# Kernel optimization log

Hardware: AMD Instinct MI355X
Metric: run time of the kernel (lower is better)

The kernel has to match this reference:

```python
import jax, jax.numpy as jnp
import numpy as np

B, D, H, K, V, M = 64, 4096, 32, 128, 128, 4096


def setup_inputs() -> dict:
    key = jax.random.key(0)
    ks = jax.random.split(key, 7)
    return {
        "x": jax.random.normal(ks[0], (B, D), dtype=jnp.float32),
        "prev_K": jax.random.normal(ks[1], (B, M, K), dtype=jnp.float32),
        "prev_V": jax.random.normal(ks[2], (B, M, V), dtype=jnp.float32),
        "P_q": jax.random.normal(ks[3], (H, D, K), dtype=jnp.float32),
        "P_k": jax.random.normal(ks[4], (D, K), dtype=jnp.float32),
        "P_v": jax.random.normal(ks[5], (D, V), dtype=jnp.float32),
        "P_o": jax.random.normal(ks[6], (H, D, V), dtype=jnp.float32),
    }


def reference(x, prev_K, prev_V, P_q, P_k, P_v, P_o):
    # Per-head query projection: [b,d] x [h,d,k] -> [b,h,k]
    q = jnp.einsum('bd,hdk->bhk', x, P_q)
    # Single shared K/V head (multi-query): append new token to cache along m
    new_k = jnp.einsum('bd,dk->bk', x, P_k)  # [b,k]
    new_v = jnp.einsum('bd,dv->bv', x, P_v)  # [b,v]
    Kc = jnp.concatenate([prev_K, new_k[:, None, :]], axis=1)  # [b,m+1,k]
    Vc = jnp.concatenate([prev_V, new_v[:, None, :]], axis=1)  # [b,m+1,v]
    # Attention over cache
    logits = jnp.einsum('bhk,bmk->bhm', q, Kc)
    weights = jax.nn.softmax(logits, axis=-1)
    O = jnp.einsum('bhm,bmv->bhv', weights, Vc)
    # Output projection: [b,h,v] x [h,d,v] -> [b,d]
    y = jnp.einsum('bhv,hdv->bd', O, P_o)
    return (y, Kc, Vc)
```

## Files before the change

### kernel.cpp

```cpp
#include <hip/hip_runtime.h>
#include <math.h>

#define Bb 64
#define Dd 4096
#define Hh 32
#define Kk 128
#define Vv 128
#define Mm 4096
#define MC 4097
#define NCH 16
#define NSLOT 17

#define WS_K1P  0
#define WS_Q    4456448
#define WS_NEWK (WS_Q + Bb*Hh*Kk)
#define WS_NEWV (WS_NEWK + Bb*Kk)
#define WS_PM   (WS_NEWV + Bb*Vv)
#define WS_PL   (WS_PM + Bb*NSLOT*Hh)
#define WS_PO   (WS_PL + Bb*NSLOT*Hh)
#define WS_O    (WS_PO + Bb*NSLOT*Hh*Vv)
#define WS_YP   (WS_O + Bb*Hh*Vv)

#define YSLOT (Bb*Dd)

#define OUT_Y  0
#define OUT_KC (Bb*Dd)
#define OUT_VC (OUT_KC + Bb*MC*Kk)

__global__ __launch_bounds__(256) void k1A_proj(const float* __restrict__ x,
        const float* __restrict__ Pq, const float* __restrict__ Pk,
        const float* __restrict__ Pv, float* __restrict__ part) {
    const int hidx = blockIdx.x;
    const int d0c  = blockIdx.y * 256;
    const int t = threadIdx.x;
    const int kg = t & 15, bg = t >> 4;
    const int kd = kg * 4, b0 = bg * 4;

    const float* P;
    if (hidx < Hh)       P = Pq + (size_t)hidx * Dd * Kk;
    else if (hidx == Hh) P = Pk;
    else                 P = Pv;

    __shared__ float xs[32 * 65];
    __shared__ float ps[32 * 128];

    float acc[4][8];
    #pragma unroll
    for (int a = 0; a < 4; a++)
        #pragma unroll
        for (int c = 0; c < 8; c++) acc[a][c] = 0.f;

    for (int tt = 0; tt < 8; tt++) {
        const int d0 = d0c + tt * 32;
        #pragma unroll
        for (int ii = 0; ii < 8; ii++) {
            int f = ii * 256 + t;
            int i = f & 31, bb = f >> 5;
            xs[i * 65 + bb] = x[(size_t)bb * Dd + d0 + i];
        }
        #pragma unroll
        for (int ii = 0; ii < 4; ii++) {
            int f = ii * 256 + t;
            int i = f >> 5, k4 = (f & 31) * 4;
            *(float4*)&ps[i * 128 + k4] = *(const float4*)&P[(size_t)(d0 + i) * Kk + k4];
        }
        __syncthreads();
        #pragma unroll
        for (int i = 0; i < 32; i++) {
            float xb[4];
            #pragma unroll
            for (int a = 0; a < 4; a++) xb[a] = xs[i * 65 + b0 + a];
            float4 p0 = *(float4*)&ps[i * 128 + kd];
            float4 p1 = *(float4*)&ps[i * 128 + 64 + kd];
            float pp[8] = {p0.x, p0.y, p0.z, p0.w, p1.x, p1.y, p1.z, p1.w};
            #pragma unroll
            for (int a = 0; a < 4; a++)
                #pragma unroll
                for (int c = 0; c < 8; c++)
                    acc[a][c] = fmaf(xb[a], pp[c], acc[a][c]);
        }
        __syncthreads();
    }
    float* dst = part + ((size_t)hidx * 16 + blockIdx.y) * 8192;
    #pragma unroll
    for (int a = 0; a < 4; a++) {
        int b = b0 + a;
        *(float4*)&dst[b * 128 + kd]      = make_float4(acc[a][0], acc[a][1], acc[a][2], acc[a][3]);
        *(float4*)&dst[b * 128 + 64 + kd] = make_float4(acc[a][4], acc[a][5], acc[a][6], acc[a][7]);
    }
}

__global__ __launch_bounds__(256) void k1B_reduce(const float* __restrict__ part,
        float* __restrict__ ws) {
    const int o = blockIdx.x * 256 + threadIdx.x;
    const int hidx = o >> 13;
    const int rest = o & 8191;
    float s = 0.f;
    #pragma unroll
    for (int c = 0; c < 16; c++) s += part[((size_t)hidx * 16 + c) * 8192 + rest];
    if (hidx < Hh) {
        int b = rest >> 7, k = rest & 127;
        ws[WS_Q + ((size_t)b * Hh + hidx) * Kk + k] = s;
    } else if (hidx == Hh) {
        ws[WS_NEWK + rest] = s;
    } else {
        ws[WS_NEWV + rest] = s;
    }
}

__global__ __launch_bounds__(256) void kflash(const float* __restrict__ prevK,
        const float* __restrict__ prevV, const float* __restrict__ wq,
        float* __restrict__ outKc, float* __restrict__ outVc,
        float* __restrict__ PM, float* __restrict__ PL, float* __restrict__ PO) {
    const int c = blockIdx.x;
    const int b = blockIdx.y;
    const int t = threadIdx.x;
    const int hg = t >> 4, lg = t & 15;
    const int h2 = hg * 2;

    __shared__ float ks_t[64 * 64];
    __shared__ float vs[64 * 132];
    __shared__ float qs[128 * 34];
    __shared__ float wl_t[64 * 36];

    {
        const int h = t >> 3, kc = t & 7;
        const float* qr = wq + ((size_t)b * Hh + h) * Kk + kc * 16;
        float4 a0 = *(const float4*)&qr[0];
        float4 a1 = *(const float4*)&qr[4];
        float4 a2 = *(const float4*)&qr[8];
        float4 a3 = *(const float4*)&qr[12];
        const int k0 = kc * 16;
        qs[(k0+ 0)*34 + h] = a0.x; qs[(k0+ 1)*34 + h] = a0.y;
        qs[(k0+ 2)*34 + h] = a0.z; qs[(k0+ 3)*34 + h] = a0.w;
        qs[(k0+ 4)*34 + h] = a1.x; qs[(k0+ 5)*34 + h] = a1.y;
        qs[(k0+ 6)*34 + h] = a1.z; qs[(k0+ 7)*34 + h] = a1.w;
        qs[(k0+ 8)*34 + h] = a2.x; qs[(k0+ 9)*34 + h] = a2.y;
        qs[(k0+10)*34 + h] = a2.z; qs[(k0+11)*34 + h] = a2.w;
        qs[(k0+12)*34 + h] = a3.x; qs[(k0+13)*34 + h] = a3.y;
        qs[(k0+14)*34 + h] = a3.z; qs[(k0+15)*34 + h] = a3.w;
    }

    float rm[2] = {-3.0e38f, -3.0e38f};
    float rl[2] = {0.f, 0.f};
    float accO[2][8] = {};
    const int kq = t & 15;
    const int vq = t & 31;

    for (int st = 0; st < 4; st++) {
        const int m0 = c * 256 + st * 64;
        __syncthreads();
        float4 kreg[8], vreg[8];
        #pragma unroll
        for (int ii = 0; ii < 4; ii++) {
            int mm = (t >> 4) + ii * 16;
            const float* src = prevK + ((size_t)b * Mm + m0 + mm) * Kk + kq * 4;
            kreg[ii]     = *(const float4*)src;
            kreg[ii + 4] = *(const float4*)(src + 64);
        }
        #pragma unroll
        for (int ii = 0; ii < 8; ii++) {
            int mm = (t >> 5) + ii * 8;
            vreg[ii] = *(const float4*)(prevV + ((size_t)b * Mm + m0 + mm) * Vv + vq * 4);
        }
        #pragma unroll
        for (int ii = 0; ii < 4; ii++) {
            int mm = (t >> 4) + ii * 16;
            int cs = (mm + 4 * kq) & 63;
            ks_t[(kq*4+0)*64 + cs] = kreg[ii].x;
            ks_t[(kq*4+1)*64 + cs] = kreg[ii].y;
            ks_t[(kq*4+2)*64 + cs] = kreg[ii].z;
            ks_t[(kq*4+3)*64 + cs] = kreg[ii].w;
        }
        #pragma unroll
        for (int ii = 0; ii < 8; ii++) {
            int mm = (t >> 5) + ii * 8;
            *(float4*)&vs[mm * 132 + vq * 4] = vreg[ii];
        }
        __syncthreads();
        #pragma unroll
        for (int ii = 0; ii < 4; ii++) {
            int mm = (t >> 4) + ii * 16;
            float* dstK = outKc + ((size_t)b * MC + m0 + mm) * Kk + kq * 4;
            *(float4*)dstK        = kreg[ii];
            *(float4*)(dstK + 64) = kreg[ii + 4];
        }
        #pragma unroll
        for (int ii = 0; ii < 8; ii++) {
            int mm = (t >> 5) + ii * 8;
            *(float4*)(outVc + ((size_t)b * MC + m0 + mm) * Vv + vq * 4) = vreg[ii];
        }
        float s[2][4] = {};
        #pragma unroll 4
        for (int k = 0; k < 64; k++) {
            float2 q2 = *(float2*)&qs[k * 34 + h2];
            float4 k4 = *(float4*)&ks_t[k * 64 + ((4*lg + 4*(k>>2)) & 63)];
            s[0][0] = fmaf(q2.x, k4.x, s[0][0]); s[0][1] = fmaf(q2.x, k4.y, s[0][1]);
            s[0][2] = fmaf(q2.x, k4.z, s[0][2]); s[0][3] = fmaf(q2.x, k4.w, s[0][3]);
            s[1][0] = fmaf(q2.y, k4.x, s[1][0]); s[1][1] = fmaf(q2.y, k4.y, s[1][1]);
            s[1][2] = fmaf(q2.y, k4.z, s[1][2]); s[1][3] = fmaf(q2.y, k4.w, s[1][3]);
        }
        __syncthreads();
        #pragma unroll
        for (int ii = 0; ii < 4; ii++) {
            int mm = (t >> 4) + ii * 16;
            int cs = (mm + 4 * kq) & 63;
            ks_t[(kq*4+0)*64 + cs] = kreg[ii+4].x;
            ks_t[(kq*4+1)*64 + cs] = kreg[ii+4].y;
            ks_t[(kq*4+2)*64 + cs] = kreg[ii+4].z;
            ks_t[(kq*4+3)*64 + cs] = kreg[ii+4].w;
        }
        __syncthreads();
        #pragma unroll 4
        for (int k = 0; k < 64; k++) {
            float2 q2 = *(float2*)&qs[(64 + k) * 34 + h2];
            float4 k4 = *(float4*)&ks_t[k * 64 + ((4*lg + 4*(k>>2)) & 63)];
            s[0][0] = fmaf(q2.x, k4.x, s[0][0]); s[0][1] = fmaf(q2.x, k4.y, s[0][1]);
            s[0][2] = fmaf(q2.x, k4.z, s[0][2]); s[0][3] = fmaf(q2.x, k4.w, s[0][3]);
            s[1][0] = fmaf(q2.y, k4.x, s[1][0]); s[1][1] = fmaf(q2.y, k4.y, s[1][1]);
            s[1][2] = fmaf(q2.y, k4.z, s[1][2]); s[1][3] = fmaf(q2.y, k4.w, s[1][3]);
        }
        float al[2];
        #pragma unroll
        for (int a = 0; a < 2; a++) {
            float mloc = fmaxf(fmaxf(s[a][0], s[a][1]), fmaxf(s[a][2], s[a][3]));
            mloc = fmaxf(mloc, __shfl_xor(mloc, 1, 64));
            mloc = fmaxf(mloc, __shfl_xor(mloc, 2, 64));
            mloc = fmaxf(mloc, __shfl_xor(mloc, 4, 64));
            mloc = fmaxf(mloc, __shfl_xor(mloc, 8, 64));
            float nm = fmaxf(rm[a], mloc);
            al[a] = __expf(rm[a] - nm);
            float psum = 0.f;
            #pragma unroll
            for (int cc = 0; cc < 4; cc++) {
                float p = __expf(s[a][cc] - nm);
                wl_t[(4*lg + cc) * 36 + h2 + a] = p;
                psum += p;
            }
            psum += __shfl_xor(psum, 1, 64);
            psum += __shfl_xor(psum, 2, 64);
            psum += __shfl_xor(psum, 4, 64);
            psum += __shfl_xor(psum, 8, 64);
            rl[a] = rl[a] * al[a] + psum;
            rm[a] = nm;
        }
        #pragma unroll
        for (int a = 0; a < 2; a++)
            #pragma unroll
            for (int j = 0; j < 8; j++) accO[a][j] *= al[a];
        for (int mm = 0; mm < 64; mm++) {
            float2 w2 = *(float2*)&wl_t[mm * 36 + h2];
            float4 v0 = *(float4*)&vs[mm * 132 + 4 * lg];
            float4 v1 = *(float4*)&vs[mm * 132 + 64 + 4 * lg];
            accO[0][0] = fmaf(w2.x, v0.x, accO[0][0]);
            accO[0][1] = fmaf(w2.x, v0.y, accO[0][1]);
            accO[0][2] = fmaf(w2.x, v0.z, accO[0][2]);
            accO[0][3] = fmaf(w2.x, v0.w, accO[0][3]);
            accO[0][4] = fmaf(w2.x, v1.x, accO[0][4]);
            accO[0][5] = fmaf(w2.x, v1.y, accO[0][5]);
            accO[0][6] = fmaf(w2.x, v1.z, accO[0][6]);
            accO[0][7] = fmaf(w2.x, v1.w, accO[0][7]);
            accO[1][0] = fmaf(w2.y, v0.x, accO[1][0]);
            accO[1][1] = fmaf(w2.y, v0.y, accO[1][1]);
            accO[1][2] = fmaf(w2.y, v0.z, accO[1][2]);
            accO[1][3] = fmaf(w2.y, v0.w, accO[1][3]);
            accO[1][4] = fmaf(w2.y, v1.x, accO[1][4]);
            accO[1][5] = fmaf(w2.y, v1.y, accO[1][5]);
            accO[1][6] = fmaf(w2.y, v1.z, accO[1][6]);
            accO[1][7] = fmaf(w2.y, v1.w, accO[1][7]);
        }
    }
    const size_t base = ((size_t)b * NSLOT + c) * Hh;
    if (lg == 0) {
        PM[base + h2]     = rm[0];
        PM[base + h2 + 1] = rm[1];
        PL[base + h2]     = rl[0];
        PL[base + h2 + 1] = rl[1];
    }
    #pragma unroll
    for (int a = 0; a < 2; a++) {
        float* po = PO + (base + h2 + a) * Vv;
        *(float4*)&po[4*lg]      = make_float4(accO[a][0], accO[a][1], accO[a][2], accO[a][3]);
        *(float4*)&po[64 + 4*lg] = make_float4(accO[a][4], accO[a][5], accO[a][6], accO[a][7]);
    }
}

__global__ __launch_bounds__(128) void knew(const float* __restrict__ ws,
        float* __restrict__ outKc, float* __restrict__ outVc,
        float* __restrict__ PM, float* __restrict__ PL, float* __restrict__ PO) {
    const int b = blockIdx.x, t = threadIdx.x;
    const float* q    = ws + WS_Q;
    const float* newk = ws + WS_NEWK;
    const float* newv = ws + WS_NEWV;
    const int h = t >> 2, j = t & 3;
    const float* qr = q + ((size_t)b * Hh + h) * Kk + j * 32;
    const float* nk = newk + (size_t)b * Kk + j * 32;
    float s0 = 0.f, s1 = 0.f, s2 = 0.f, s3 = 0.f;
    #pragma unroll
    for (int i = 0; i < 8; i++) {
        float4 a  = *(const float4*)&qr[i * 4];
        float4 c4 = *(const float4*)&nk[i * 4];
        s0 = fmaf(a.x, c4.x, s0); s1 = fmaf(a.y, c4.y, s1);
        s2 = fmaf(a.z, c4.z, s2); s3 = fmaf(a.w, c4.w, s3);
    }
    float s = (s0 + s1) + (s2 + s3);
    s += __shfl_xor(s, 1, 64);
    s += __shfl_xor(s, 2, 64);
    const size_t base = ((size_t)b * NSLOT + 16) * Hh;
    if (j == 0) { PM[base + h] = s; PL[base + h] = 1.f; }
    float nv = newv[(size_t)b * Vv + t];
    outKc[((size_t)b * MC + Mm) * Kk + t] = newk[(size_t)b * Kk + t];
    outVc[((size_t)b * MC + Mm) * Vv + t] = nv;
    #pragma unroll 4
    for (int hh = 0; hh < Hh; hh++)
        PO[(base + hh) * Vv + t] = nv;
}

__global__ __launch_bounds__(128) void kcomb(const float* __restrict__ PM,
        const float* __restrict__ PL, const float* __restrict__ PO,
        float* __restrict__ O) {
    const int h = blockIdx.x, b = blockIdx.y, t = threadIdx.x;
    __shared__ float ml[NSLOT], ll[NSLOT];
    if (t < NSLOT) {
        ml[t] = PM[((size_t)b * NSLOT + t) * Hh + h];
        ll[t] = PL[((size_t)b * NSLOT + t) * Hh + h];
    }
    __syncthreads();
    float M = -3.0e38f;
    #pragma unroll
    for (int c = 0; c < NSLOT; c++) M = fmaxf(M, ml[c]);
    float L = 0.f, o = 0.f;
    #pragma unroll
    for (int c = 0; c < NSLOT; c++) {
        float e = __expf(ml[c] - M);
        L += ll[c] * e;
        o = fmaf(e, PO[(((size_t)b * NSLOT + c) * Hh + h) * Vv + t], o);
    }
    O[((size_t)b * Hh + h) * Vv + t] = o / L;
}

__global__ __launch_bounds__(256) void k5_outproj(const float* __restrict__ O,
        const float* __restrict__ Po, float* __restrict__ ypart) {
    const int dbase = blockIdx.x * 64;
    const int hq = blockIdx.y;
    const int t = threadIdx.x;
    __shared__ float os[64 * 64];
    __shared__ float ps2[64 * 64];
    const int dg = t & 15, bg = t >> 4;
    const int d0 = dg * 4, b0 = bg * 4;
    float acc[4][4] = {};
    for (int hi = 0; hi < 4; hi++) {
        const int h = hq * 4 + hi;
        for (int vh = 0; vh < 2; vh++) {
            __syncthreads();
            #pragma unroll
            for (int ii = 0; ii < 4; ii++) {
                int f = ii * 256 + t;
                int vq2 = f & 15, r = f >> 4;
                int colp = (4 * vq2 + 4 * (r >> 2)) & 63;
                *(float4*)&os[r * 64 + colp] =
                    *(const float4*)&O[((size_t)(r * Hh + h)) * Vv + vh * 64 + 4 * vq2];
// ... 67 lines not shown
```

Baseline: 252.9 us.

## Double-buffer K/V register prefetch in flash kernel and halve chunk count

Each flash block now processes 512 cache rows in eight stages instead of 256 rows in four. The stage loop is fully unrolled through macros with two register buffers, so the next stage's K/V global loads are issued while the current stage computes. Launch bounds request two blocks per SM, and the partial-slot count drops from 17 to 9, which shrinks the combine work. The costs are higher register pressure, possible spills from holding two float4[8] buffers per thread, and half as many blocks (64x8), which lowers parallelism across the GPU.

```diff
diff --git a/kernel.cpp b/kernel.cpp
--- a/kernel.cpp
+++ b/kernel.cpp
@@ -8,8 +8,8 @@
 #define Vv 128
 #define Mm 4096
 #define MC 4097
-#define NCH 16
-#define NSLOT 17
+#define NCH 8
+#define NSLOT 9
 
 #define WS_K1P  0
 #define WS_Q    4456448
@@ -108,7 +108,133 @@
     }
 }
 
-__global__ __launch_bounds__(256) void kflash(const float* __restrict__ prevK,
+#define LOADKV(ST, KR, VR) { \
+    const int m0_ = c * 512 + (ST) * 64; \
+    _Pragma("unroll") \
+    for (int ii = 0; ii < 4; ii++) { \
+        int mm = mK + ii * 16; \
+        const float* src = prevK + ((size_t)b * Mm + m0_ + mm) * Kk + kq * 4; \
+        KR[ii]     = *(const float4*)src; \
+        KR[ii + 4] = *(const float4*)(src + 64); \
+    } \
+    _Pragma("unroll") \
+    for (int ii = 0; ii < 8; ii++) { \
+        int mm = mV + ii * 8; \
+        VR[ii] = *(const float4*)(prevV + ((size_t)b * Mm + m0_ + mm) * Vv + vq * 4); \
+    } }
+
+#define FLASH_BODY(KC, VC, KN, VN, ST, PRE) { \
+    const int m0_ = c * 512 + (ST) * 64; \
+    __syncthreads();                          \
+    _Pragma("unroll") \
+    for (int ii = 0; ii < 4; ii++) {          \
+        int mm = mK + ii * 16; \
+        int cs = (mm + 4 * kq) & 63; \
+        ks_t[(kq*4+0)*64 + cs] = KC[ii].x; \
+        ks_t[(kq*4+1)*64 + cs] = KC[ii].y; \
+        ks_t[(kq*4+2)*64 + cs] = KC[ii].z; \
+        ks_t[(kq*4+3)*64 + cs] = KC[ii].w; \
+    } \
+    _Pragma("unroll") \
+    for (int ii = 0; ii < 8; ii++) {          \
+        int mm = mV + ii * 8; \
+        *(float4*)&vs[mm * 132 + vq * 4] = VC[ii]; \
+    } \
+    __syncthreads();                          \
+    if (PRE) LOADKV((ST) + 1, KN, VN);        \
+    _Pragma("unroll") \
+    for (int ii = 0; ii < 4; ii++) {          \
+        int mm = mK + ii * 16; \
+        float* dK = outKc + ((size_t)b * MC + m0_ + mm) * Kk + kq * 4; \
+        *(float4*)dK        = KC[ii]; \
+        *(float4*)(dK + 64) = KC[ii + 4]; \
+    } \
+    _Pragma("unroll") \
+    for (int ii = 0; ii < 8; ii++) {          \
+        int mm = mV + ii * 8; \
+        *(float4*)(outVc + ((size_t)b * MC + m0_ + mm) * Vv + vq * 4) = VC[ii]; \
+    } \
+    float s[2][4] = {{0.f,0.f,0.f,0.f},{0.f,0.f,0.f,0.f}}; \
+    _Pragma("unroll 4") \
+    for (int k = 0; k < 64; k++) {            \
+        float2 q2 = *(float2*)&qs[k * 34 + h2]; \
+        float4 k4 = *(float4*)&ks_t[k * 64 + ((4*lg + 4*(k>>2)) & 63)]; \
+        s[0][0] = fmaf(q2.x, k4.x, s[0][0]); s[0][1] = fmaf(q2.x, k4.y, s[0][1]); \
+        s[0][2] = fmaf(q2.x, k4.z, s[0][2]); s[0][3] = fmaf(q2.x, k4.w, s[0][3]); \
+        s[1][0] = fmaf(q2.y, k4.x, s[1][0]); s[1][1] = fmaf(q2.y, k4.y, s[1][1]); \
+        s[1][2] = fmaf(q2.y, k4.z, s[1][2]); s[1][3] = fmaf(q2.y, k4.w, s[1][3]); \
+    } \
+    __syncthreads();                          \
+    _Pragma("unroll") \
+    for (int ii = 0; ii < 4; ii++) {          \
+        int mm = mK + ii * 16; \
+        int cs = (mm + 4 * kq) & 63; \
+        ks_t[(kq*4+0)*64 + cs] = KC[ii+4].x; \
+        ks_t[(kq*4+1)*64 + cs] = KC[ii+4].y; \
+        ks_t[(kq*4+2)*64 + cs] = KC[ii+4].z; \
+        ks_t[(kq*4+3)*64 + cs] = KC[ii+4].w; \
+    } \
+    __syncthreads();                          \
+    _Pragma("unroll 4") \
+    for (int k = 0; k < 64; k++) {            \
+        float2 q2 = *(float2*)&qs[(64 + k) * 34 + h2]; \
+        float4 k4 = *(float4*)&ks_t[k * 64 + ((4*lg + 4*(k>>2)) & 63)]; \
+        s[0][0] = fmaf(q2.x, k4.x, s[0][0]); s[0][1] = fmaf(q2.x, k4.y, s[0][1]); \
+        s[0][2] = fmaf(q2.x, k4.z, s[0][2]); s[0][3] = fmaf(q2.x, k4.w, s[0][3]); \
+        s[1][0] = fmaf(q2.y, k4.x, s[1][0]); s[1][1] = fmaf(q2.y, k4.y, s[1][1]); \
+        s[1][2] = fmaf(q2.y, k4.z, s[1][2]); s[1][3] = fmaf(q2.y, k4.w, s[1][3]); \
+    } \
+    float al[2]; \
+    _Pragma("unroll") \
+    for (int a = 0; a < 2; a++) {             \
+        float mloc = fmaxf(fmaxf(s[a][0], s[a][1]), fmaxf(s[a][2], s[a][3])); \
+        mloc = fmaxf(mloc, __shfl_xor(mloc, 1, 64)); \
+        mloc = fmaxf(mloc, __shfl_xor(mloc, 2, 64)); \
+        mloc = fmaxf(mloc, __shfl_xor(mloc, 4, 64)); \
+        mloc = fmaxf(mloc, __shfl_xor(mloc, 8, 64)); \
+        float nm = fmaxf(rm[a], mloc); \
+        al[a] = __expf(rm[a] - nm); \
+        float psum = 0.f; \
+        _Pragma("unroll") \
+        for (int cc = 0; cc < 4; cc++) { \
+            float p = __expf(s[a][cc] - nm); \
+            wl_t[(4*lg + cc) * 36 + h2 + a] = p; \
+            psum += p; \
+        } \
+        psum += __shfl_xor(psum, 1, 64); \
+        psum += __shfl_xor(psum, 2, 64); \
+        psum += __shfl_xor(psum, 4, 64); \
+        psum += __shfl_xor(psum, 8, 64); \
+        rl[a] = rl[a] * al[a] + psum; \
+        rm[a] = nm; \
+    } \
+    _Pragma("unroll") \
+    for (int a = 0; a < 2; a++) \
+        _Pragma("unroll") \
+        for (int j = 0; j < 8; j++) accO[a][j] *= al[a]; \
+    for (int mm = 0; mm < 64; mm++) {         \
+        float2 w2 = *(float2*)&wl_t[mm * 36 + h2]; \
+        float4 v0 = *(float4*)&vs[mm * 132 + 4 * lg]; \
+        float4 v1 = *(float4*)&vs[mm * 132 + 64 + 4 * lg]; \
+        accO[0][0] = fmaf(w2.x, v0.x, accO[0][0]); \
+        accO[0][1] = fmaf(w2.x, v0.y, accO[0][1]); \
+        accO[0][2] = fmaf(w2.x, v0.z, accO[0][2]); \
+        accO[0][3] = fmaf(w2.x, v0.w, accO[0][3]); \
+        accO[0][4] = fmaf(w2.x, v1.x, accO[0][4]); \
+        accO[0][5] = fmaf(w2.x, v1.y, accO[0][5]); \
+        accO[0][6] = fmaf(w2.x, v1.z, accO[0][6]); \
+        accO[0][7] = fmaf(w2.x, v1.w, accO[0][7]); \
+        accO[1][0] = fmaf(w2.y, v0.x, accO[1][0]); \
+        accO[1][1] = fmaf(w2.y, v0.y, accO[1][1]); \
+        accO[1][2] = fmaf(w2.y, v0.z, accO[1][2]); \
+        accO[1][3] = fmaf(w2.y, v0.w, accO[1][3]); \
+        accO[1][4] = fmaf(w2.y, v1.x, accO[1][4]); \
+        accO[1][5] = fmaf(w2.y, v1.y, accO[1][5]); \
+        accO[1][6] = fmaf(w2.y, v1.z, accO[1][6]); \
+        accO[1][7] = fmaf(w2.y, v1.w, accO[1][7]); \
+    } }
+
+__global__ __launch_bounds__(256, 2) void kflash(const float* __restrict__ prevK,
         const float* __restrict__ prevV, const float* __restrict__ wq,
         float* __restrict__ outKc, float* __restrict__ outVc,
         float* __restrict__ PM, float* __restrict__ PL, float* __restrict__ PO) {
@@ -117,11 +243,18 @@
     const int t = threadIdx.x;
     const int hg = t >> 4, lg = t & 15;
     const int h2 = hg * 2;
+    const int kq = t & 15;
+    const int mK = t >> 4;
+    const int vq = t & 31;
+    const int mV = t >> 5;
 
     __shared__ float ks_t[64 * 64];
     __shared__ float vs[64 * 132];
     __shared__ float qs[128 * 34];
     __shared__ float wl_t[64 * 36];
+
+    float4 ka[8], va[8], kb[8], vb[8];
+    LOADKV(0, ka, va);
 
     {
         const int h = t >> 3, kc = t & 7;
@@ -144,132 +277,16 @@
     float rm[2] = {-3.0e38f, -3.0e38f};
     float rl[2] = {0.f, 0.f};
     float accO[2][8] = {};
-    const int kq = t & 15;
-    const int vq = t & 31;
-
-    for (int st = 0; st < 4; st++) {
-        const int m0 = c * 256 + st * 64;
-        __syncthreads();
-        float4 kreg[8], vreg[8];
-        #pragma unroll
-        for (int ii = 0; ii < 4; ii++) {
-            int mm = (t >> 4) + ii * 16;
-            const float* src = prevK + ((size_t)b * Mm + m0 + mm) * Kk + kq * 4;
-            kreg[ii]     = *(const float4*)src;
-            kreg[ii + 4] = *(const float4*)(src + 64);
-        }
-        #pragma unroll
-        for (int ii = 0; ii < 8; ii++) {
-            int mm = (t >> 5) + ii * 8;
-            vreg[ii] = *(const float4*)(prevV + ((size_t)b * Mm + m0 + mm) * Vv + vq * 4);
-        }
-        #pragma unroll
-        for (int ii = 0; ii < 4; ii++) {
-            int mm = (t >> 4) + ii * 16;
-            int cs = (mm + 4 * kq) & 63;
-            ks_t[(kq*4+0)*64 + cs] = kreg[ii].x;
-            ks_t[(kq*4+1)*64 + cs] = kreg[ii].y;
-            ks_t[(kq*4+2)*64 + cs] = kreg[ii].z;
-            ks_t[(kq*4+3)*64 + cs] = kreg[ii].w;
-        }
-        #pragma unroll
-        for (int ii = 0; ii < 8; ii++) {
-            int mm = (t >> 5) + ii * 8;
-            *(float4*)&vs[mm * 132 + vq * 4] = vreg[ii];
-        }
-        __syncthreads();
-        #pragma unroll
-        for (int ii = 0; ii < 4; ii++) {
-            int mm = (t >> 4) + ii * 16;
-            float* dstK = outKc + ((size_t)b * MC + m0 + mm) * Kk + kq * 4;
-            *(float4*)dstK        = kreg[ii];
-            *(float4*)(dstK + 64) = kreg[ii + 4];
-        }
-        #pragma unroll
-        for (int ii = 0; ii < 8; ii++) {
-            int mm = (t >> 5) + ii * 8;
-            *(float4*)(outVc + ((size_t)b * MC + m0 + mm) * Vv + vq * 4) = vreg[ii];
-        }
-        float s[2][4] = {};
-        #pragma unroll 4
-        for (int k = 0; k < 64; k++) {
-            float2 q2 = *(float2*)&qs[k * 34 + h2];
-            float4 k4 = *(float4*)&ks_t[k * 64 + ((4*lg + 4*(k>>2)) & 63)];
-            s[0][0] = fmaf(q2.x, k4.x, s[0][0]); s[0][1] = fmaf(q2.x, k4.y, s[0][1]);
-            s[0][2] = fmaf(q2.x, k4.z, s[0][2]); s[0][3] = fmaf(q2.x, k4.w, s[0][3]);
-            s[1][0] = fmaf(q2.y, k4.x, s[1][0]); s[1][1] = fmaf(q2.y, k4.y, s[1][1]);
-            s[1][2] = fmaf(q2.y, k4.z, s[1][2]); s[1][3] = fmaf(q2.y, k4.w, s[1][3]);
-        }
-        __syncthreads();
-        #pragma unroll
-        for (int ii = 0; ii < 4; ii++) {
-            int mm = (t >> 4) + ii * 16;
-            int cs = (mm + 4 * kq) & 63;
-            ks_t[(kq*4+0)*64 + cs] = kreg[ii+4].x;
-            ks_t[(kq*4+1)*64 + cs] = kreg[ii+4].y;
-            ks_t[(kq*4+2)*64 + cs] = kreg[ii+4].z;
-            ks_t[(kq*4+3)*64 + cs] = kreg[ii+4].w;
-        }
-        __syncthreads();
-        #pragma unroll 4
-        for (int k = 0; k < 64; k++) {
-            float2 q2 = *(float2*)&qs[(64 + k) * 34 + h2];
-            float4 k4 = *(float4*)&ks_t[k * 64 + ((4*lg + 4*(k>>2)) & 63)];
-            s[0][0] = fmaf(q2.x, k4.x, s[0][0]); s[0][1] = fmaf(q2.x, k4.y, s[0][1]);
-            s[0][2] = fmaf(q2.x, k4.z, s[0][2]); s[0][3] = fmaf(q2.x, k4.w, s[0][3]);
-            s[1][0] = fmaf(q2.y, k4.x, s[1][0]); s[1][1] = fmaf(q2.y, k4.y, s[1][1]);
-            s[1][2] = fmaf(q2.y, k4.z, s[1][2]); s[1][3] = fmaf(q2.y, k4.w, s[1][3]);
-        }
-        float al[2];
-        #pragma unroll
-        for (int a = 0; a < 2; a++) {
-            float mloc = fmaxf(fmaxf(s[a][0], s[a][1]), fmaxf(s[a][2], s[a][3]));
-            mloc = fmaxf(mloc, __shfl_xor(mloc, 1, 64));
-            mloc = fmaxf(mloc, __shfl_xor(mloc, 2, 64));
-            mloc = fmaxf(mloc, __shfl_xor(mloc, 4, 64));
-            mloc = fmaxf(mloc, __shfl_xor(mloc, 8, 64));
-            float nm = fmaxf(rm[a], mloc);
-            al[a] = __expf(rm[a] - nm);
-            float psum = 0.f;
-            #pragma unroll
-            for (int cc = 0; cc < 4; cc++) {
-                float p = __expf(s[a][cc] - nm);
-                wl_t[(4*lg + cc) * 36 + h2 + a] = p;
-                psum += p;
-            }
-            psum += __shfl_xor(psum, 1, 64);
-            psum += __shfl_xor(psum, 2, 64);
-            psum += __shfl_xor(psum, 4, 64);
-            psum += __shfl_xor(psum, 8, 64);
-            rl[a] = rl[a] * al[a] + psum;
-            rm[a] = nm;
-        }
-        #pragma unroll
-        for (int a = 0; a < 2; a++)
-            #pragma unroll
-            for (int j = 0; j < 8; j++) accO[a][j] *= al[a];
-        for (int mm = 0; mm < 64; mm++) {
-            float2 w2 = *(float2*)&wl_t[mm * 36 + h2];
-            float4 v0 = *(float4*)&vs[mm * 132 + 4 * lg];
-            float4 v1 = *(float4*)&vs[mm * 132 + 64 + 4 * lg];
-            accO[0][0] = fmaf(w2.x, v0.x, accO[0][0]);
-            accO[0][1] = fmaf(w2.x, v0.y, accO[0][1]);
-            accO[0][2] = fmaf(w2.x, v0.z, accO[0][2]);
-            accO[0][3] = fmaf(w2.x, v0.w, accO[0][3]);
-            accO[0][4] = fmaf(w2.x, v1.x, accO[0][4]);
-            accO[0][5] = fmaf(w2.x, v1.y, accO[0][5]);
-            accO[0][6] = fmaf(w2.x, v1.z, accO[0][6]);
-            accO[0][7] = fmaf(w2.x, v1.w, accO[0][7]);
-            accO[1][0] = fmaf(w2.y, v0.x, accO[1][0]);
-            accO[1][1] = fmaf(w2.y, v0.y, accO[1][1]);
-            accO[1][2] = fmaf(w2.y, v0.z, accO[1][2]);
-            accO[1][3] = fmaf(w2.y, v0.w, accO[1][3]);
-            accO[1][4] = fmaf(w2.y, v1.x, accO[1][4]);
-            accO[1][5] = fmaf(w2.y, v1.y, accO[1][5]);
-            accO[1][6] = fmaf(w2.y, v1.z, accO[1][6]);
-            accO[1][7] = fmaf(w2.y, v1.w, accO[1][7]);
-        }
-    }
+
+    FLASH_BODY(ka, va, kb, vb, 0, true)
+    FLASH_BODY(kb, vb, ka, va, 1, true)
+    FLASH_BODY(ka, va, kb, vb, 2, true)
+    FLASH_BODY(kb, vb, ka, va, 3, true)
+    FLASH_BODY(ka, va, kb, vb, 4, true)
+    FLASH_BODY(kb, vb, ka, va, 5, true)
+    FLASH_BODY(ka, va, kb, vb, 6, true)
+    FLASH_BODY(kb, vb, ka, va, 7, false)
+
     const size_t base = ((size_t)b * NSLOT + c) * Hh;
     if (lg == 0) {
         PM[base + h2]     = rm[0];
@@ -306,7 +323,7 @@
     float s = (s0 + s1) + (s2 + s3);
     s += __shfl_xor(s, 1, 64);
     s += __shfl_xor(s, 2, 64);
-    const size_t base = ((size_t)b * NSLOT + 16) * Hh;
+    const size_t base = ((size_t)b * NSLOT + NCH) * Hh;
     if (j == 0) { PM[base + h] = s; PL[base + h] = 1.f; }
     float nv = newv[(size_t)b * Vv + t];
     outKc[((size_t)b * MC + Mm) * Kk + t] = newk[(size_t)b * Kk + t];
```

Result: slower. 287.5 us (+13.7%).

## Halve kflash LDS tiles and stage K/V in 32-row chunks for occupancy

Applied to the files above, without the earlier changes.

The K and V shared-memory staging buffers in kflash shrink to half size. K is now staged as four 32-wide k slices, each followed by its partial QK dot product, and V as two 32-row halves, each followed by its partial PV accumulation. Launch bounds now request 3 blocks per SM. The aim is to cut LDS use per block so more blocks stay resident and hide global memory latency. In exchange, each 64-row step gets several extra __syncthreads barriers, and register pressure under the stricter launch bound may cause spills.

```diff
diff --git a/kernel.cpp b/kernel.cpp
--- a/kernel.cpp
+++ b/kernel.cpp
@@ -108,7 +108,57 @@
     }
 }
 
-__global__ __launch_bounds__(256) void kflash(const float* __restrict__ prevK,
+
+#define WRITEK(SEL, OFF) { \
+    if ((kq >> 3) == (SEL)) { \
+        const int kq7 = kq & 7; \
+        _Pragma("unroll") \
+        for (int ii = 0; ii < 4; ii++) { \
+            int mm = mK + ii * 16; \
+            int cs = (mm + 4 * kq7) & 63; \
+            ks_t[(4*kq7+0)*64 + cs] = ka[ii+(OFF)].x; \
+            ks_t[(4*kq7+1)*64 + cs] = ka[ii+(OFF)].y; \
+            ks_t[(4*kq7+2)*64 + cs] = ka[ii+(OFF)].z; \
+            ks_t[(4*kq7+3)*64 + cs] = ka[ii+(OFF)].w; \
+        } \
+    } }
+
+#define QKQ(KB) { \
+    _Pragma("unroll 8") \
+    for (int r = 0; r < 32; r++) { \
+        float2 q2 = *(float2*)&qs[((KB) + r) * 34 + h2]; \
+        float4 k4 = *(float4*)&ks_t[r * 64 + ((4*lg + 4*(r>>2)) & 63)]; \
+        s[0][0] = fmaf(q2.x, k4.x, s[0][0]); s[0][1] = fmaf(q2.x, k4.y, s[0][1]); \
+        s[0][2] = fmaf(q2.x, k4.z, s[0][2]); s[0][3] = fmaf(q2.x, k4.w, s[0][3]); \
+        s[1][0] = fmaf(q2.y, k4.x, s[1][0]); s[1][1] = fmaf(q2.y, k4.y, s[1][1]); \
+        s[1][2] = fmaf(q2.y, k4.z, s[1][2]); s[1][3] = fmaf(q2.y, k4.w, s[1][3]); \
+    } }
+
+#define PVH(MB) { \
+    _Pragma("unroll 4") \
+    for (int mm = 0; mm < 32; mm++) { \
+        float2 w2 = *(float2*)&wl_t[((MB) + mm) * 36 + h2]; \
+        float4 v0 = *(float4*)&vs[mm * 132 + 4 * lg]; \
+        float4 v1 = *(float4*)&vs[mm * 132 + 64 + 4 * lg]; \
+        accO[0][0] = fmaf(w2.x, v0.x, accO[0][0]); \
+        accO[0][1] = fmaf(w2.x, v0.y, accO[0][1]); \
+        accO[0][2] = fmaf(w2.x, v0.z, accO[0][2]); \
+        accO[0][3] = fmaf(w2.x, v0.w, accO[0][3]); \
+        accO[0][4] = fmaf(w2.x, v1.x, accO[0][4]); \
+        accO[0][5] = fmaf(w2.x, v1.y, accO[0][5]); \
+        accO[0][6] = fmaf(w2.x, v1.z, accO[0][6]); \
+        accO[0][7] = fmaf(w2.x, v1.w, accO[0][7]); \
+        accO[1][0] = fmaf(w2.y, v0.x, accO[1][0]); \
+        accO[1][1] = fmaf(w2.y, v0.y, accO[1][1]); \
+        accO[1][2] = fmaf(w2.y, v0.z, accO[1][2]); \
+        accO[1][3] = fmaf(w2.y, v0.w, accO[1][3]); \
+        accO[1][4] = fmaf(w2.y, v1.x, accO[1][4]); \
+        accO[1][5] = fmaf(w2.y, v1.y, accO[1][5]); \
+        accO[1][6] = fmaf(w2.y, v1.z, accO[1][6]); \
+        accO[1][7] = fmaf(w2.y, v1.w, accO[1][7]); \
+    } }
+
+__global__ __launch_bounds__(256, 3) void kflash(const float* __restrict__ prevK,
         const float* __restrict__ prevV, const float* __restrict__ wq,
         float* __restrict__ outKc, float* __restrict__ outVc,
         float* __restrict__ PM, float* __restrict__ PL, float* __restrict__ PO) {
@@ -117,9 +167,13 @@
     const int t = threadIdx.x;
     const int hg = t >> 4, lg = t & 15;
     const int h2 = hg * 2;
-
-    __shared__ float ks_t[64 * 64];
-    __shared__ float vs[64 * 132];
+    const int kq = t & 15;
+    const int mK = t >> 4;
+    const int vq = t & 31;
+    const int mV = t >> 5;
+
+    __shared__ float ks_t[32 * 64];
+    __shared__ float vs[32 * 132];
     __shared__ float qs[128 * 34];
     __shared__ float wl_t[64 * 36];
 
@@ -144,82 +198,54 @@
     float rm[2] = {-3.0e38f, -3.0e38f};
     float rl[2] = {0.f, 0.f};
     float accO[2][8] = {};
-    const int kq = t & 15;
-    const int vq = t & 31;
 
     for (int st = 0; st < 4; st++) {
         const int m0 = c * 256 + st * 64;
         __syncthreads();
-        float4 kreg[8], vreg[8];
+        float4 ka[8], va[8];
         #pragma unroll
         for (int ii = 0; ii < 4; ii++) {
-            int mm = (t >> 4) + ii * 16;
+            int mm = mK + ii * 16;
             const float* src = prevK + ((size_t)b * Mm + m0 + mm) * Kk + kq * 4;
-            kreg[ii]     = *(const float4*)src;
-            kreg[ii + 4] = *(const float4*)(src + 64);
+            ka[ii]     = *(const float4*)src;
+            ka[ii + 4] = *(const float4*)(src + 64);
         }
         #pragma unroll
         for (int ii = 0; ii < 8; ii++) {
-            int mm = (t >> 5) + ii * 8;
-            vreg[ii] = *(const float4*)(prevV + ((size_t)b * Mm + m0 + mm) * Vv + vq * 4);
-        }
+            int mm = mV + ii * 8;
+            va[ii] = *(const float4*)(prevV + ((size_t)b * Mm + m0 + mm) * Vv + vq * 4);
+        }
+        #pragma unroll
+        for (int ii = 0; ii < 4; ii++)
+            *(float4*)&vs[(mV + ii * 8) * 132 + vq * 4] = va[ii];
+        WRITEK(0, 0)
+        __syncthreads();
         #pragma unroll
         for (int ii = 0; ii < 4; ii++) {
-            int mm = (t >> 4) + ii * 16;
-            int cs = (mm + 4 * kq) & 63;
-            ks_t[(kq*4+0)*64 + cs] = kreg[ii].x;
-            ks_t[(kq*4+1)*64 + cs] = kreg[ii].y;
-            ks_t[(kq*4+2)*64 + cs] = kreg[ii].z;
-            ks_t[(kq*4+3)*64 + cs] = kreg[ii].w;
+            int mm = mK + ii * 16;
+            float* dK = outKc + ((size_t)b * MC + m0 + mm) * Kk + kq * 4;
+            *(float4*)dK        = ka[ii];
+            *(float4*)(dK + 64) = ka[ii + 4];
         }
         #pragma unroll
         for (int ii = 0; ii < 8; ii++) {
-            int mm = (t >> 5) + ii * 8;
-            *(float4*)&vs[mm * 132 + vq * 4] = vreg[ii];
-        }
-        __syncthreads();
-        #pragma unroll
-        for (int ii = 0; ii < 4; ii++) {
-            int mm = (t >> 4) + ii * 16;
-            float* dstK = outKc + ((size_t)b * MC + m0 + mm) * Kk + kq * 4;
-            *(float4*)dstK        = kreg[ii];
-            *(float4*)(dstK + 64) = kreg[ii + 4];
-        }
-        #pragma unroll
-        for (int ii = 0; ii < 8; ii++) {
-            int mm = (t >> 5) + ii * 8;
-            *(float4*)(outVc + ((size_t)b * MC + m0 + mm) * Vv + vq * 4) = vreg[ii];
-        }
-        float s[2][4] = {};
-        #pragma unroll 4
-        for (int k = 0; k < 64; k++) {
-            float2 q2 = *(float2*)&qs[k * 34 + h2];
-            float4 k4 = *(float4*)&ks_t[k * 64 + ((4*lg + 4*(k>>2)) & 63)];
-            s[0][0] = fmaf(q2.x, k4.x, s[0][0]); s[0][1] = fmaf(q2.x, k4.y, s[0][1]);
-            s[0][2] = fmaf(q2.x, k4.z, s[0][2]); s[0][3] = fmaf(q2.x, k4.w, s[0][3]);
-            s[1][0] = fmaf(q2.y, k4.x, s[1][0]); s[1][1] = fmaf(q2.y, k4.y, s[1][1]);
-            s[1][2] = fmaf(q2.y, k4.z, s[1][2]); s[1][3] = fmaf(q2.y, k4.w, s[1][3]);
-        }
-        __syncthreads();
-        #pragma unroll
-        for (int ii = 0; ii < 4; ii++) {
-            int mm = (t >> 4) + ii * 16;
-            int cs = (mm + 4 * kq) & 63;
-            ks_t[(kq*4+0)*64 + cs] = kreg[ii+4].x;
-            ks_t[(kq*4+1)*64 + cs] = kreg[ii+4].y;
-            ks_t[(kq*4+2)*64 + cs] = kreg[ii+4].z;
-            ks_t[(kq*4+3)*64 + cs] = kreg[ii+4].w;
-        }
-        __syncthreads();
-        #pragma unroll 4
-        for (int k = 0; k < 64; k++) {
-            float2 q2 = *(float2*)&qs[(64 + k) * 34 + h2];
-            float4 k4 = *(float4*)&ks_t[k * 64 + ((4*lg + 4*(k>>2)) & 63)];
-            s[0][0] = fmaf(q2.x, k4.x, s[0][0]); s[0][1] = fmaf(q2.x, k4.y, s[0][1]);
-            s[0][2] = fmaf(q2.x, k4.z, s[0][2]); s[0][3] = fmaf(q2.x, k4.w, s[0][3]);
-            s[1][0] = fmaf(q2.y, k4.x, s[1][0]); s[1][1] = fmaf(q2.y, k4.y, s[1][1]);
-            s[1][2] = fmaf(q2.y, k4.z, s[1][2]); s[1][3] = fmaf(q2.y, k4.w, s[1][3]);
-        }
+            int mm = mV + ii * 8;
+            *(float4*)(outVc + ((size_t)b * MC + m0 + mm) * Vv + vq * 4) = va[ii];
+        }
+        float s[2][4] = {{0.f,0.f,0.f,0.f},{0.f,0.f,0.f,0.f}};
+        QKQ(0)
+        __syncthreads();
+        WRITEK(1, 0)
+        __syncthreads();
+        QKQ(32)
+        __syncthreads();
+        WRITEK(0, 4)
+        __syncthreads();
+        QKQ(64)
+        __syncthreads();
+        WRITEK(1, 4)
+        __syncthreads();
+        QKQ(96)
         float al[2];
         #pragma unroll
         for (int a = 0; a < 2; a++) {
@@ -248,27 +274,13 @@
         for (int a = 0; a < 2; a++)
             #pragma unroll
             for (int j = 0; j < 8; j++) accO[a][j] *= al[a];
-        for (int mm = 0; mm < 64; mm++) {
-            float2 w2 = *(float2*)&wl_t[mm * 36 + h2];
-            float4 v0 = *(float4*)&vs[mm * 132 + 4 * lg];
-            float4 v1 = *(float4*)&vs[mm * 132 + 64 + 4 * lg];
-            accO[0][0] = fmaf(w2.x, v0.x, accO[0][0]);
-            accO[0][1] = fmaf(w2.x, v0.y, accO[0][1]);
-            accO[0][2] = fmaf(w2.x, v0.z, accO[0][2]);
-            accO[0][3] = fmaf(w2.x, v0.w, accO[0][3]);
-            accO[0][4] = fmaf(w2.x, v1.x, accO[0][4]);
-            accO[0][5] = fmaf(w2.x, v1.y, accO[0][5]);
-            accO[0][6] = fmaf(w2.x, v1.z, accO[0][6]);
-            accO[0][7] = fmaf(w2.x, v1.w, accO[0][7]);
-            accO[1][0] = fmaf(w2.y, v0.x, accO[1][0]);
-            accO[1][1] = fmaf(w2.y, v0.y, accO[1][1]);
-            accO[1][2] = fmaf(w2.y, v0.z, accO[1][2]);
-            accO[1][3] = fmaf(w2.y, v0.w, accO[1][3]);
-            accO[1][4] = fmaf(w2.y, v1.x, accO[1][4]);
-            accO[1][5] = fmaf(w2.y, v1.y, accO[1][5]);
-            accO[1][6] = fmaf(w2.y, v1.z, accO[1][6]);
-            accO[1][7] = fmaf(w2.y, v1.w, accO[1][7]);
-        }
+        PVH(0)
+        __syncthreads();
+        #pragma unroll
+        for (int ii = 0; ii < 4; ii++)
+            *(float4*)&vs[(mV + ii * 8) * 132 + vq * 4] = va[ii + 4];
+        __syncthreads();
+        PVH(32)
     }
     const size_t base = ((size_t)b * NSLOT + c) * Hh;
     if (lg == 0) {
@@ -306,7 +318,7 @@
     float s = (s0 + s1) + (s2 + s3);
     s += __shfl_xor(s, 1, 64);
     s += __shfl_xor(s, 2, 64);
-    const size_t base = ((size_t)b * NSLOT + 16) * Hh;
+    const size_t base = ((size_t)b * NSLOT + NCH) * Hh;
     if (j == 0) { PM[base + h] = s; PL[base + h] = 1.f; }
     float nv = newv[(size_t)b * Vv + t];
     outKc[((size_t)b * MC + Mm) * Kk + t] = newk[(size_t)b * Kk + t];
```

Measured after the change: 285.5 us. 12.9% more time.

## Retile flash attention kernel with 4x4 register blocks and split-K score reduction

Applied to the files above, without the earlier changes.

Reworks the thread mapping in the attention chunk kernel so each thread computes a 4-head by 4-position score tile. The key dimension is split across thread pairs and the partials are combined through shared memory. The PV stage uses 4 heads by 4 value columns per thread, and V is staged in two 32-row halves to shrink LDS. It also moves the Kc/Vc output stores before the first barrier and uses custom barriers that wait only on LDS counters. This raises register-level reuse of LDS loads, at the cost of more barriers and an extra reduction step.

```diff
diff --git a/kernel.cpp b/kernel.cpp
--- a/kernel.cpp
+++ b/kernel.cpp
@@ -27,6 +27,13 @@
 #define OUT_KC (Bb*Dd)
 #define OUT_VC (OUT_KC + Bb*MC*Kk)
 
+#define BAR_LGKM() do { \
+    __builtin_amdgcn_sched_barrier(0); \
+    asm volatile("s_waitcnt lgkmcnt(0)" ::: "memory"); \
+    __builtin_amdgcn_s_barrier(); \
+    __builtin_amdgcn_sched_barrier(0); \
+} while (0)
+
 __global__ __launch_bounds__(256) void k1A_proj(const float* __restrict__ x,
         const float* __restrict__ Pq, const float* __restrict__ Pk,
         const float* __restrict__ Pv, float* __restrict__ part) {
@@ -115,13 +122,19 @@
     const int c = blockIdx.x;
     const int b = blockIdx.y;
     const int t = threadIdx.x;
-    const int hg = t >> 4, lg = t & 15;
-    const int h2 = hg * 2;
+    const int kq = t & 15, mKl = t >> 4;
+    const int vq = t & 31, mVl = t >> 5;
+    const int kg = t & 1;
+    const int mg = (t >> 1) & 15;
+    const int hq = t >> 5;
+    const int vg = t & 31;
 
     __shared__ float ks_t[64 * 64];
-    __shared__ float vs[64 * 132];
-    __shared__ float qs[128 * 34];
-    __shared__ float wl_t[64 * 36];
+    __shared__ float vs[32 * 132];
+    __shared__ float qs[128 * 36];
+    __shared__ float wl[64 * 36];
+    __shared__ float scb[32 * 64];
+    __shared__ float als[32];
 
     {
         const int h = t >> 3, kc = t & 7;
@@ -131,158 +144,212 @@
         float4 a2 = *(const float4*)&qr[8];
         float4 a3 = *(const float4*)&qr[12];
         const int k0 = kc * 16;
-        qs[(k0+ 0)*34 + h] = a0.x; qs[(k0+ 1)*34 + h] = a0.y;
-        qs[(k0+ 2)*34 + h] = a0.z; qs[(k0+ 3)*34 + h] = a0.w;
-        qs[(k0+ 4)*34 + h] = a1.x; qs[(k0+ 5)*34 + h] = a1.y;
-        qs[(k0+ 6)*34 + h] = a1.z; qs[(k0+ 7)*34 + h] = a1.w;
-        qs[(k0+ 8)*34 + h] = a2.x; qs[(k0+ 9)*34 + h] = a2.y;
-        qs[(k0+10)*34 + h] = a2.z; qs[(k0+11)*34 + h] = a2.w;
-        qs[(k0+12)*34 + h] = a3.x; qs[(k0+13)*34 + h] = a3.y;
-        qs[(k0+14)*34 + h] = a3.z; qs[(k0+15)*34 + h] = a3.w;
-    }
-
-    float rm[2] = {-3.0e38f, -3.0e38f};
-    float rl[2] = {0.f, 0.f};
-    float accO[2][8] = {};
-    const int kq = t & 15;
-    const int vq = t & 31;
+        qs[(k0+ 0)*36 + h] = a0.x; qs[(k0+ 1)*36 + h] = a0.y;
+        qs[(k0+ 2)*36 + h] = a0.z; qs[(k0+ 3)*36 + h] = a0.w;
+        qs[(k0+ 4)*36 + h] = a1.x; qs[(k0+ 5)*36 + h] = a1.y;
+        qs[(k0+ 6)*36 + h] = a1.z; qs[(k0+ 7)*36 + h] = a1.w;
+        qs[(k0+ 8)*36 + h] = a2.x; qs[(k0+ 9)*36 + h] = a2.y;
+        qs[(k0+10)*36 + h] = a2.z; qs[(k0+11)*36 + h] = a2.w;
+        qs[(k0+12)*36 + h] = a3.x; qs[(k0+13)*36 + h] = a3.y;
+        qs[(k0+14)*36 + h] = a3.z; qs[(k0+15)*36 + h] = a3.w;
+    }
+
+    float rm[4] = {-3.0e38f, -3.0e38f, -3.0e38f, -3.0e38f};
+    float rl[4] = {0.f, 0.f, 0.f, 0.f};
+    float acc[4][4];
+    #pragma unroll
+    for (int a = 0; a < 4; a++)
+        #pragma unroll
+        for (int cc = 0; cc < 4; cc++) acc[a][cc] = 0.f;
 
     for (int st = 0; st < 4; st++) {
         const int m0 = c * 256 + st * 64;
-        __syncthreads();
-        float4 kreg[8], vreg[8];
+        BAR_LGKM();
+        float4 ka[8], va[8];
         #pragma unroll
         for (int ii = 0; ii < 4; ii++) {
-            int mm = (t >> 4) + ii * 16;
+            int mm = mKl + ii * 16;
             const float* src = prevK + ((size_t)b * Mm + m0 + mm) * Kk + kq * 4;
-            kreg[ii]     = *(const float4*)src;
-            kreg[ii + 4] = *(const float4*)(src + 64);
+            ka[ii]     = *(const float4*)src;
+            ka[ii + 4] = *(const float4*)(src + 64);
         }
         #pragma unroll
         for (int ii = 0; ii < 8; ii++) {
-            int mm = (t >> 5) + ii * 8;
-            vreg[ii] = *(const float4*)(prevV + ((size_t)b * Mm + m0 + mm) * Vv + vq * 4);
-        }
+            int mm = mVl + ii * 8;
+            va[ii] = *(const float4*)(prevV + ((size_t)b * Mm + m0 + mm) * Vv + vq * 4);
+        }
+        #pragma unroll
+        for (int ii = 0; ii < 4; ii++)
+            *(float4*)&vs[(mVl + ii * 8) * 132 + vq * 4] = va[ii];
         #pragma unroll
         for (int ii = 0; ii < 4; ii++) {
-            int mm = (t >> 4) + ii * 16;
+            int mm = mKl + ii * 16;
             int cs = (mm + 4 * kq) & 63;
-            ks_t[(kq*4+0)*64 + cs] = kreg[ii].x;
-            ks_t[(kq*4+1)*64 + cs] = kreg[ii].y;
-            ks_t[(kq*4+2)*64 + cs] = kreg[ii].z;
-            ks_t[(kq*4+3)*64 + cs] = kreg[ii].w;
+            ks_t[(kq*4+0)*64 + cs] = ka[ii].x;
+            ks_t[(kq*4+1)*64 + cs] = ka[ii].y;
+            ks_t[(kq*4+2)*64 + cs] = ka[ii].z;
+            ks_t[(kq*4+3)*64 + cs] = ka[ii].w;
+        }
+        #pragma unroll
+        for (int ii = 0; ii < 4; ii++) {
+            int mm = mKl + ii * 16;
+            float* dK = outKc + ((size_t)b * MC + m0 + mm) * Kk + kq * 4;
+            *(float4*)dK        = ka[ii];
+            *(float4*)(dK + 64) = ka[ii + 4];
         }
         #pragma unroll
         for (int ii = 0; ii < 8; ii++) {
-            int mm = (t >> 5) + ii * 8;
-            *(float4*)&vs[mm * 132 + vq * 4] = vreg[ii];
-        }
-        __syncthreads();
+            int mm = mVl + ii * 8;
+            *(float4*)(outVc + ((size_t)b * MC + m0 + mm) * Vv + vq * 4) = va[ii];
+        }
+        BAR_LGKM();
+        float s[4][4];
+        #pragma unroll
+        for (int a = 0; a < 4; a++)
+            #pragma unroll
+            for (int cc = 0; cc < 4; cc++) s[a][cc] = 0.f;
+        #pragma unroll 8
+        for (int j = 0; j < 32; j++) {
+            int rk = kg * 32 + j;
+            float4 q4 = *(float4*)&qs[rk * 36 + hq * 4];
+            int kc = (mg * 4 + 4 * (rk >> 2)) & 63;
+            float4 k4 = *(float4*)&ks_t[rk * 64 + kc];
+            #pragma unroll
+            for (int a = 0; a < 4; a++) {
+                float qa = (a==0)?q4.x:(a==1)?q4.y:(a==2)?q4.z:q4.w;
+                s[a][0] = fmaf(qa, k4.x, s[a][0]);
+                s[a][1] = fmaf(qa, k4.y, s[a][1]);
+                s[a][2] = fmaf(qa, k4.z, s[a][2]);
+                s[a][3] = fmaf(qa, k4.w, s[a][3]);
+            }
+        }
+        BAR_LGKM();
         #pragma unroll
         for (int ii = 0; ii < 4; ii++) {
-            int mm = (t >> 4) + ii * 16;
-            float* dstK = outKc + ((size_t)b * MC + m0 + mm) * Kk + kq * 4;
-            *(float4*)dstK        = kreg[ii];
-            *(float4*)(dstK + 64) = kreg[ii + 4];
-        }
-        #pragma unroll
-        for (int ii = 0; ii < 8; ii++) {
-            int mm = (t >> 5) + ii * 8;
-            *(float4*)(outVc + ((size_t)b * MC + m0 + mm) * Vv + vq * 4) = vreg[ii];
-        }
-        float s[2][4] = {};
-        #pragma unroll 4
-        for (int k = 0; k < 64; k++) {
-            float2 q2 = *(float2*)&qs[k * 34 + h2];
-            float4 k4 = *(float4*)&ks_t[k * 64 + ((4*lg + 4*(k>>2)) & 63)];
-            s[0][0] = fmaf(q2.x, k4.x, s[0][0]); s[0][1] = fmaf(q2.x, k4.y, s[0][1]);
-            s[0][2] = fmaf(q2.x, k4.z, s[0][2]); s[0][3] = fmaf(q2.x, k4.w, s[0][3]);
-            s[1][0] = fmaf(q2.y, k4.x, s[1][0]); s[1][1] = fmaf(q2.y, k4.y, s[1][1]);
-            s[1][2] = fmaf(q2.y, k4.z, s[1][2]); s[1][3] = fmaf(q2.y, k4.w, s[1][3]);
-        }
-        __syncthreads();
-        #pragma unroll
-        for (int ii = 0; ii < 4; ii++) {
-            int mm = (t >> 4) + ii * 16;
+            int mm = mKl + ii * 16;
             int cs = (mm + 4 * kq) & 63;
-            ks_t[(kq*4+0)*64 + cs] = kreg[ii+4].x;
-            ks_t[(kq*4+1)*64 + cs] = kreg[ii+4].y;
-            ks_t[(kq*4+2)*64 + cs] = kreg[ii+4].z;
-            ks_t[(kq*4+3)*64 + cs] = kreg[ii+4].w;
-        }
-        __syncthreads();
-        #pragma unroll 4
-        for (int k = 0; k < 64; k++) {
-            float2 q2 = *(float2*)&qs[(64 + k) * 34 + h2];
-            float4 k4 = *(float4*)&ks_t[k * 64 + ((4*lg + 4*(k>>2)) & 63)];
-            s[0][0] = fmaf(q2.x, k4.x, s[0][0]); s[0][1] = fmaf(q2.x, k4.y, s[0][1]);
-            s[0][2] = fmaf(q2.x, k4.z, s[0][2]); s[0][3] = fmaf(q2.x, k4.w, s[0][3]);
-            s[1][0] = fmaf(q2.y, k4.x, s[1][0]); s[1][1] = fmaf(q2.y, k4.y, s[1][1]);
-            s[1][2] = fmaf(q2.y, k4.z, s[1][2]); s[1][3] = fmaf(q2.y, k4.w, s[1][3]);
-        }
-        float al[2];
-        #pragma unroll
-        for (int a = 0; a < 2; a++) {
+            ks_t[(kq*4+0)*64 + cs] = ka[ii+4].x;
+            ks_t[(kq*4+1)*64 + cs] = ka[ii+4].y;
+            ks_t[(kq*4+2)*64 + cs] = ka[ii+4].z;
+            ks_t[(kq*4+3)*64 + cs] = ka[ii+4].w;
+        }
+        BAR_LGKM();
+        #pragma unroll 8
+        for (int j = 0; j < 32; j++) {
+            int rk = kg * 32 + j;
+            float4 q4 = *(float4*)&qs[(64 + rk) * 36 + hq * 4];
+            int kc = (mg * 4 + 4 * (rk >> 2)) & 63;
+            float4 k4 = *(float4*)&ks_t[rk * 64 + kc];
+            #pragma unroll
+            for (int a = 0; a < 4; a++) {
+                float qa = (a==0)?q4.x:(a==1)?q4.y:(a==2)?q4.z:q4.w;
+                s[a][0] = fmaf(qa, k4.x, s[a][0]);
+                s[a][1] = fmaf(qa, k4.y, s[a][1]);
+                s[a][2] = fmaf(qa, k4.z, s[a][2]);
+                s[a][3] = fmaf(qa, k4.w, s[a][3]);
+            }
+        }
+        if (kg) {
+            #pragma unroll
+            for (int a = 0; a < 4; a++)
+                *(float4*)&scb[(hq*4 + a) * 64 + mg * 4] =
+                    make_float4(s[a][0], s[a][1], s[a][2], s[a][3]);
+        }
+        BAR_LGKM();
+        if (!kg) {
+            #pragma unroll
+            for (int a = 0; a < 4; a++) {
+                float4 pp = *(float4*)&scb[(hq*4 + a) * 64 + mg * 4];
+                s[a][0] += pp.x; s[a][1] += pp.y; s[a][2] += pp.z; s[a][3] += pp.w;
+            }
+        }
+        float p[4][4];
+        float al4[4];
+        #pragma unroll
+        for (int a = 0; a < 4; a++) {
             float mloc = fmaxf(fmaxf(s[a][0], s[a][1]), fmaxf(s[a][2], s[a][3]));
-            mloc = fmaxf(mloc, __shfl_xor(mloc, 1, 64));
             mloc = fmaxf(mloc, __shfl_xor(mloc, 2, 64));
             mloc = fmaxf(mloc, __shfl_xor(mloc, 4, 64));
             mloc = fmaxf(mloc, __shfl_xor(mloc, 8, 64));
+            mloc = fmaxf(mloc, __shfl_xor(mloc, 16, 64));
             float nm = fmaxf(rm[a], mloc);
-            al[a] = __expf(rm[a] - nm);
+            al4[a] = __expf(rm[a] - nm);
             float psum = 0.f;
             #pragma unroll
             for (int cc = 0; cc < 4; cc++) {
-                float p = __expf(s[a][cc] - nm);
-                wl_t[(4*lg + cc) * 36 + h2 + a] = p;
-                psum += p;
-            }
-            psum += __shfl_xor(psum, 1, 64);
+                p[a][cc] = __expf(s[a][cc] - nm);
+                psum += p[a][cc];
+            }
             psum += __shfl_xor(psum, 2, 64);
             psum += __shfl_xor(psum, 4, 64);
             psum += __shfl_xor(psum, 8, 64);
-            rl[a] = rl[a] * al[a] + psum;
+            psum += __shfl_xor(psum, 16, 64);
+            rl[a] = rl[a] * al4[a] + psum;
             rm[a] = nm;
         }
-        #pragma unroll
-        for (int a = 0; a < 2; a++)
-            #pragma unroll
-            for (int j = 0; j < 8; j++) accO[a][j] *= al[a];
-        for (int mm = 0; mm < 64; mm++) {
-            float2 w2 = *(float2*)&wl_t[mm * 36 + h2];
-            float4 v0 = *(float4*)&vs[mm * 132 + 4 * lg];
-            float4 v1 = *(float4*)&vs[mm * 132 + 64 + 4 * lg];
-            accO[0][0] = fmaf(w2.x, v0.x, accO[0][0]);
-            accO[0][1] = fmaf(w2.x, v0.y, accO[0][1]);
-            accO[0][2] = fmaf(w2.x, v0.z, accO[0][2]);
-            accO[0][3] = fmaf(w2.x, v0.w, accO[0][3]);
-            accO[0][4] = fmaf(w2.x, v1.x, accO[0][4]);
-            accO[0][5] = fmaf(w2.x, v1.y, accO[0][5]);
-            accO[0][6] = fmaf(w2.x, v1.z, accO[0][6]);
-            accO[0][7] = fmaf(w2.x, v1.w, accO[0][7]);
-            accO[1][0] = fmaf(w2.y, v0.x, accO[1][0]);
-            accO[1][1] = fmaf(w2.y, v0.y, accO[1][1]);
-            accO[1][2] = fmaf(w2.y, v0.z, accO[1][2]);
-            accO[1][3] = fmaf(w2.y, v0.w, accO[1][3]);
-            accO[1][4] = fmaf(w2.y, v1.x, accO[1][4]);
-            accO[1][5] = fmaf(w2.y, v1.y, accO[1][5]);
-            accO[1][6] = fmaf(w2.y, v1.z, accO[1][6]);
-            accO[1][7] = fmaf(w2.y, v1.w, accO[1][7]);
+        if (!kg) {
+            #pragma unroll
+            for (int cc = 0; cc < 4; cc++)
+                *(float4*)&wl[(mg*4 + cc) * 36 + hq * 4] =
+                    make_float4(p[0][cc], p[1][cc], p[2][cc], p[3][cc]);
+            if (mg == 0) {
+                #pragma unroll
+                for (int a = 0; a < 4; a++) als[hq*4 + a] = al4[a];
+            }
+        }
+        BAR_LGKM();
+        {
+            float4 a4 = *(float4*)&als[hq * 4];
+            float aa[4] = {a4.x, a4.y, a4.z, a4.w};
+            #pragma unroll
+            for (int a = 0; a < 4; a++)
+                #pragma unroll
+                for (int cc = 0; cc < 4; cc++) acc[a][cc] *= aa[a];
+        }
+        #pragma unroll 8
+        for (int m = 0; m < 32; m++) {
+            float4 w4 = *(float4*)&wl[m * 36 + hq * 4];
+            float4 v4 = *(float4*)&vs[m * 132 + vg * 4];
+            #pragma unroll
+            for (int a = 0; a < 4; a++) {
+                float wa = (a==0)?w4.x:(a==1)?w4.y:(a==2)?w4.z:w4.w;
+                acc[a][0] = fmaf(wa, v4.x, acc[a][0]);
+                acc[a][1] = fmaf(wa, v4.y, acc[a][1]);
+                acc[a][2] = fmaf(wa, v4.z, acc[a][2]);
+                acc[a][3] = fmaf(wa, v4.w, acc[a][3]);
+            }
+        }
+        BAR_LGKM();
+        #pragma unroll
+        for (int ii = 0; ii < 4; ii++)
+            *(float4*)&vs[(mVl + ii * 8) * 132 + vq * 4] = va[ii + 4];
+        BAR_LGKM();
+        #pragma unroll 8
+        for (int m = 0; m < 32; m++) {
+            float4 w4 = *(float4*)&wl[(32 + m) * 36 + hq * 4];
+            float4 v4 = *(float4*)&vs[m * 132 + vg * 4];
+            #pragma unroll
+            for (int a = 0; a < 4; a++) {
+                float wa = (a==0)?w4.x:(a==1)?w4.y:(a==2)?w4.z:w4.w;
+                acc[a][0] = fmaf(wa, v4.x, acc[a][0]);
+                acc[a][1] = fmaf(wa, v4.y, acc[a][1]);
+                acc[a][2] = fmaf(wa, v4.z, acc[a][2]);
+                acc[a][3] = fmaf(wa, v4.w, acc[a][3]);
+            }
         }
     }
     const size_t base = ((size_t)b * NSLOT + c) * Hh;
-    if (lg == 0) {
-        PM[base + h2]     = rm[0];
-        PM[base + h2 + 1] = rm[1];
-        PL[base + h2]     = rl[0];
-        PL[base + h2 + 1] = rl[1];
-    }
-    #pragma unroll
-    for (int a = 0; a < 2; a++) {
-        float* po = PO + (base + h2 + a) * Vv;
-        *(float4*)&po[4*lg]      = make_float4(accO[a][0], accO[a][1], accO[a][2], accO[a][3]);
-        *(float4*)&po[64 + 4*lg] = make_float4(accO[a][4], accO[a][5], accO[a][6], accO[a][7]);
-    }
+    if (kg == 0 && mg == 0) {
+        #pragma unroll
+        for (int a = 0; a < 4; a++) {
+            PM[base + hq*4 + a] = rm[a];
+            PL[base + hq*4 + a] = rl[a];
+        }
+    }
+    #pragma unroll
+    for (int a = 0; a < 4; a++)
+        *(float4*)&PO[(base + hq*4 + a) * Vv + vg * 4] =
+            make_float4(acc[a][0], acc[a][1], acc[a][2], acc[a][3]);
 }
 
 __global__ __launch_bounds__(128) void knew(const float* __restrict__ ws,
@@ -306,7 +373,7 @@
     float s = (s0 + s1) + (s2 + s3);
     s += __shfl_xor(s, 1, 64);
     s += __shfl_xor(s, 2, 64);
-    const size_t base = ((size_t)b * NSLOT + 16) * Hh;
+    const size_t base = ((size_t)b * NSLOT + NCH) * Hh;
     if (j == 0) { PM[base + h] = s; PL[base + h] = 1.f; }
     float nv = newv[(size_t)b * Vv + t];
     outKc[((size_t)b * MC + Mm) * Kk + t] = newk[(size_t)b * Kk + t];
```

After: 253.3 us. About the same (+0.2%).
